# Optimization experiments

Hardware: AMD Instinct MI355X
Metric: run time of the kernel (lower is better)

## Reference

```python
import jax, jax.numpy as jnp
import numpy as np

N = 8192
E_DIM = 256
HID = 256
OUT = 128
N_PRED = 2_000_000


def setup_inputs() -> dict:
    key = jax.random.key(0)
    ks = jax.random.split(key, 6)
    node_indices = jnp.arange(N, dtype=jnp.int64) if jax.config.jax_enable_x64 else jnp.arange(N, dtype=jnp.int32)
    attn_matrix = jax.random.normal(ks[0], (N, N), dtype=jnp.float32)
    edge_label_index = jax.random.randint(ks[1], (2, N_PRED), 0, N)
    emb = jax.random.normal(ks[2], (N, E_DIM), dtype=jnp.float32) * 0.05
    W1 = jax.random.normal(ks[3], (E_DIM, HID), dtype=jnp.float32) * (1.0 / np.sqrt(E_DIM))
    b1 = jnp.zeros((HID,), dtype=jnp.float32)
    W2 = jax.random.normal(ks[4], (HID, OUT), dtype=jnp.float32) * (1.0 / np.sqrt(HID))
    b2 = jnp.zeros((OUT,), dtype=jnp.float32)
    return {"node_indices": node_indices, "attn_matrix": attn_matrix,
            "edge_label_index": edge_label_index, "emb": emb,
            "W1": W1, "b1": b1, "W2": W2, "b2": b2}


def reference(node_indices, attn_matrix, edge_label_index, emb, W1, b1, W2, b2):
    # dense_to_sparse of an (almost surely) all-nonzero dense matrix keeps all
    # N^2 edges (incl. diagonal), so no extra self-loops are added by gcn_norm.
    w = jax.nn.relu(attn_matrix)                       # edge weights after F.relu
    deg = w.sum(axis=0)                                # deg[j] = sum_i w[i,j] (scatter on col)
    dis = jnp.where(deg > 0, jax.lax.rsqrt(deg), 0.0)  # deg^{-1/2}, inf -> 0
    a_norm = dis[:, None] * w * dis[None, :]           # norm_ij = d_i^-1/2 w_ij d_j^-1/2

    x = emb[node_indices]                              # embedding lookup [N, E_DIM]
    # GCNConv: aggregate transformed features at target (col): out = A_norm^T @ (x W) + b
    h = jax.nn.relu(a_norm.T @ (x @ W1) + b1)          # [N, HID]
    z = a_norm.T @ (h @ W2) + b2                       # [N, OUT]

    # decode: dot product between endpoint embeddings
    scores = jnp.einsum('ed,ed->e', z[edge_label_index[0]], z[edge_label_index[1]])
    return scores
```

## Files before the change

kernel.cpp:

```cpp
#include <hip/hip_runtime.h>

typedef _Float16 half8  __attribute__((ext_vector_type(8)));
typedef _Float16 half4v __attribute__((ext_vector_type(4)));
typedef _Float16 half2v __attribute__((ext_vector_type(2)));
typedef float    floatx4 __attribute__((ext_vector_type(4)));
typedef float    f4v     __attribute__((ext_vector_type(4)));

#define NND 8192
#define PA  40
#define PT  128

__device__ __forceinline__ int swzk(int m, int k) { return k ^ (((m >> 3) & 3) << 3); }
__device__ __forceinline__ int swzT(int row, int chunk) { return chunk ^ ((row >> 2) & 15); }

#define GLOAD16(gp, lp) __builtin_amdgcn_global_load_lds(                        \
    (const __attribute__((address_space(1))) void*)(gp),                         \
    (__attribute__((address_space(3))) void*)(lp), 16, 0, 0)

#define VMCNT0() asm volatile("s_waitcnt vmcnt(0)" ::: "memory")

__device__ __forceinline__ float dis_of(float d) { return d > 0.f ? 1.f / sqrtf(d) : 0.f; }

__global__ __launch_bounds__(256) void k_degT(const float* __restrict__ A,
                                              _Float16* __restrict__ Wh,
                                              float* __restrict__ deg) {
    __shared__ _Float16 T[128 * PT];
    __shared__ float sdeg[8 * 128];
    int t  = threadIdx.x;
    int j0 = blockIdx.x * 128, i0 = blockIdx.y * 128;
    int c = t & 31;
    int g = t >> 5;

    f4v s = {0.f, 0.f, 0.f, 0.f};
    #pragma unroll
    for (int p = 0; p < 2; ++p) {
        int rb = 64 * p + 8 * g;
        f4v v[8];
        #pragma unroll
        for (int rr = 0; rr < 8; ++rr)
            v[rr] = *(const f4v*)(A + (size_t)(i0 + rb + rr) * NND + j0 + 4 * c);
        #pragma unroll
        for (int rr = 0; rr < 8; ++rr)
            #pragma unroll
            for (int u = 0; u < 4; ++u) v[rr][u] = fmaxf(v[rr][u], 0.f);
        #pragma unroll
        for (int u = 0; u < 4; ++u) {
            half8 hv;
            #pragma unroll
            for (int rr = 0; rr < 8; ++rr) { hv[rr] = (_Float16)v[rr][u]; s[u] += v[rr][u]; }
            int row = 4 * c + u;
            int chunk = 8 * p + g;
            *(half8*)(&T[row * PT + swzT(row, chunk) * 8]) = hv;
        }
    }
    *(f4v*)(&sdeg[g * 128 + 4 * c]) = s;
    __syncthreads();

    if (t < 128) {
        float d = 0.f;
        #pragma unroll
        for (int g2 = 0; g2 < 8; ++g2) d += sdeg[g2 * 128 + t];
        atomicAdd(&deg[j0 + t], d);
    }

    #pragma unroll
    for (int p = 0; p < 8; ++p) {
        int j  = 16 * p + (t >> 4);
        int mc = t & 15;
        half8 hv = *(const half8*)(&T[j * PT + swzT(j, mc) * 8]);
        *(half8*)(Wh + (size_t)(j0 + j) * NND + i0 + mc * 8) = hv;
    }
}

template <typename AT>
__global__ __launch_bounds__(256) void k_mm_small(
    const AT* __restrict__ Abase, const int* __restrict__ gather,
    const float* __restrict__ B, int NB,
    _Float16* __restrict__ outT, const float* __restrict__ deg, float out_scale) {

    __shared__ _Float16 As[128 * PA];
    __shared__ _Float16 Bs[64 * PA];

    int t  = threadIdx.x;
    int i0 = blockIdx.x * 128;
    int n0 = blockIdx.y * 64;

    int am = t & 127, akh = t >> 7;
    int row = i0 + am;
    if (gather) row = gather[row];
    const AT* arow = Abase + (size_t)row * 256;

    int tp = t & 15, kp = t >> 4;

    int lane = t & 63, w = t >> 6;
    int wm = w & 1, wn = w >> 1;
    int lm = lane & 15, q = lane >> 4;

    floatx4 acc[4][2];
    #pragma unroll
    for (int a = 0; a < 4; ++a)
        #pragma unroll
        for (int b = 0; b < 2; ++b) acc[a][b] = (floatx4){0.f, 0.f, 0.f, 0.f};

    for (int ks = 0; ks < 8; ++ks) {
        int c0 = ks * 32;

        half8 av[2];
        if constexpr (sizeof(AT) == 4) {
            #pragma unroll
            for (int cc = 0; cc < 2; ++cc) {
                f4v v0 = *(const f4v*)(arow + c0 + akh * 16 + cc * 8);
                f4v v1 = *(const f4v*)(arow + c0 + akh * 16 + cc * 8 + 4);
                half8 hv;
                #pragma unroll
                for (int e = 0; e < 4; ++e) {
                    hv[e]     = (_Float16)(16.f * v0[e]);
                    hv[4 + e] = (_Float16)(16.f * v1[e]);
                }
                av[cc] = hv;
            }
        } else {
            av[0] = *(const half8*)(arow + c0 + akh * 16);
            av[1] = *(const half8*)(arow + c0 + akh * 16 + 8);
        }

        const float* bp = B + (size_t)(c0 + 2 * kp) * NB + n0 + 4 * tp;
        f4v r0 = *(const f4v*)bp;
        f4v r1 = *(const f4v*)(bp + NB);

        __syncthreads();
        #pragma unroll
        for (int cc = 0; cc < 2; ++cc) {
            int k = akh * 16 + cc * 8;
            *(half8*)(&As[am * PA + swzk(am, k)]) = av[cc];
        }
        #pragma unroll
        for (int u = 0; u < 4; ++u) {
            int n = 4 * tp + u;
            half2v p = {(_Float16)r0[u], (_Float16)r1[u]};
            *(half2v*)(&Bs[n * PA + swzk(n, 2 * kp)]) = p;
        }
        __syncthreads();

        half8 af[4], bf[2];
        #pragma unroll
        for (int mt = 0; mt < 4; ++mt) {
            int m = wm * 64 + mt * 16 + lm;
            af[mt] = *(const half8*)(&As[m * PA + swzk(m, q * 8)]);
        }
        #pragma unroll
        for (int nt = 0; nt < 2; ++nt) {
            int n = wn * 32 + nt * 16 + lm;
            bf[nt] = *(const half8*)(&Bs[n * PA + swzk(n, q * 8)]);
        }
        #pragma unroll
        for (int mt = 0; mt < 4; ++mt)
            #pragma unroll
            for (int nt = 0; nt < 2; ++nt)
                acc[mt][nt] = __builtin_amdgcn_mfma_f32_16x16x32_f16(af[mt], bf[nt], acc[mt][nt], 0, 0, 0);
    }

    #pragma unroll
    for (int mt = 0; mt < 4; ++mt) {
        int ib = i0 + wm * 64 + mt * 16 + q * 4;
        float di[4];
        #pragma unroll
        for (int r = 0; r < 4; ++r) di[r] = dis_of(deg[ib + r]) * out_scale;
        #pragma unroll
        for (int nt = 0; nt < 2; ++nt) {
            int n = n0 + wn * 32 + nt * 16 + lm;
            #pragma unroll
            for (int r = 0; r < 4; ++r) {
                float v = acc[mt][nt][r] * di[r];
                outT[(size_t)n * NND + ib + r] = (_Float16)v;
            }
        }
    }
}

template <int BN, int ZSTEPS>
__global__ __launch_bounds__(256) void k_mm_big(
    const _Float16* __restrict__ Wh, const _Float16* __restrict__ Bt, float* __restrict__ Cp) {

    __shared__ __align__(16) _Float16 As[2 * 128 * 32];
    __shared__ __align__(16) _Float16 Bs[2 * 128 * 32];

    int t = threadIdx.x;
    int bx = blockIdx.x;
    bx = (bx & 7) * 8 + (bx >> 3);
    int j0 = bx * 128;
    int n0 = blockIdx.y * 128;
    size_t i_begin = (size_t)blockIdx.z * (ZSTEPS * 32);
    float* C = Cp + (size_t)blockIdx.z * (size_t)NND * BN;

    int lane = t & 63, w = t >> 6;
    int wm = w & 1, wn = w >> 1;
    int lm = lane & 15, q = lane >> 4;
    int qa = q ^ ((lm >> 1) & 3);

    int srow = lane >> 2;
    int scol = ((lane & 3) ^ ((lane >> 3) & 3)) * 8;
    const _Float16* aS0 = Wh + (size_t)(j0 + w * 16 + srow) * NND + i_begin + scol;
    const _Float16* aS1 = aS0 + (size_t)64 * NND;
    const _Float16* bS0 = Bt + (size_t)(n0 + w * 16 + srow) * NND + i_begin + scol;
    const _Float16* bS1 = bS0 + (size_t)64 * NND;

    char* aLb = (char*)As + w * 1024;
    char* bLb = (char*)Bs + w * 1024;

    floatx4 acc[4][4];
    #pragma unroll
    for (int a = 0; a < 4; ++a)
        #pragma unroll
        for (int b = 0; b < 4; ++b) acc[a][b] = (floatx4){0.f, 0.f, 0.f, 0.f};

    GLOAD16(aS0, aLb);
    GLOAD16(aS1, aLb + 4096);
    GLOAD16(bS0, bLb);
    GLOAD16(bS1, bLb + 4096);
    VMCNT0();
    __builtin_amdgcn_s_barrier();

    for (int ks = 0; ks < ZSTEPS; ++ks) {
        int cur = ks & 1;
        const _Float16* Ab = As + cur * 4096;
        const _Float16* Bb = Bs + cur * 4096;

        if (ks < ZSTEPS - 1) {
            int ko = (ks + 1) * 32;
            char* aL = aLb + (cur ^ 1) * 8192;
            char* bL = bLb + (cur ^ 1) * 8192;
            GLOAD16(aS0 + ko, aL);
            GLOAD16(aS1 + ko, aL + 4096);
            GLOAD16(bS0 + ko, bL);
            GLOAD16(bS1 + ko, bL + 4096);
        }

        half8 af[4], bf[4];
        #pragma unroll
        for (int mt = 0; mt < 4; ++mt) {
            int m = wm * 64 + mt * 16 + lm;
            af[mt] = *(const half8*)(&Ab[m * 32 + qa * 8]);
        }
        #pragma unroll
        for (int nt = 0; nt < 4; ++nt) {
            int n = wn * 64 + nt * 16 + lm;
            bf[nt] = *(const half8*)(&Bb[n * 32 + qa * 8]);
        }
        __builtin_amdgcn_s_setprio(1);
        #pragma unroll
        for (int mt = 0; mt < 4; ++mt)
            #pragma unroll
            for (int nt = 0; nt < 4; ++nt)
                acc[mt][nt] = __builtin_amdgcn_mfma_f32_16x16x32_f16(af[mt], bf[nt], acc[mt][nt], 0, 0, 0);
        __builtin_amdgcn_s_setprio(0);

        VMCNT0();
        __builtin_amdgcn_s_barrier();
    }

    #pragma unroll
    for (int mt = 0; mt < 4; ++mt) {
        int rb = j0 + wm * 64 + mt * 16 + q * 4;
        #pragma unroll
        for (int nt = 0; nt < 4; ++nt) {
            int col = n0 + wn * 64 + nt * 16 + lm;
            #pragma unroll
            for (int r = 0; r < 4; ++r)
                C[(size_t)(rb + r) * BN + col] = acc[mt][nt][r];
        }
    }
}

template <int NSH, bool RELU, int NZ>
__global__ __launch_bounds__(256) void k_finalize(const float* __restrict__ Cp, const float* __restrict__ deg,
                                                  const float* __restrict__ bias, _Float16* __restrict__ out) {
    int idx4 = (blockIdx.x * 256 + threadIdx.x) * 4;
    f4v v = {0.f, 0.f, 0.f, 0.f};
    #pragma unroll
    for (int z = 0; z < NZ; ++z) {
        f4v p = *(const f4v*)(Cp + (size_t)z * (NND << NSH) + idx4);
        #pragma unroll
        for (int r = 0; r < 4; ++r) v[r] += p[r];
    }
    int j  = idx4 >> NSH;
    int n0 = idx4 & ((1 << NSH) - 1);
    float dj = dis_of(deg[j]) * (1.f / 1024.f);
    f4v b4 = *(const f4v*)(bias + n0);
    half4v o;
    #pragma unroll
    for (int r = 0; r < 4; ++r) {
        float x = v[r] * dj + b4[r];
        if (RELU) x = fmaxf(x, 0.f);
        o[r] = (_Float16)(x * 64.f);
    }
    *(half4v*)(out + idx4) = o;
}

__global__ __launch_bounds__(256) void k_edges(const _Float16* __restrict__ zh, const int* __restrict__ ei,
                                               float* __restrict__ out, int npred) {
    int g0 = ((blockIdx.x * 256 + threadIdx.x) >> 4) * 4;
    int l = threadIdx.x & 15;
    #pragma unroll
    for (int e = 0; e < 4; ++e) {
        int g = g0 + e;
        if (g >= npred) return;
        int a = ei[g], b = ei[npred + g];
        half8 za = *(const half8*)(zh + (size_t)a * 128 + l * 8);
        half8 zb = *(const half8*)(zh + (size_t)b * 128 + l * 8);
        float s = 0.f;
        #pragma unroll
        for (int u = 0; u < 4; ++u) {
            half2v a2 = {za[2 * u], za[2 * u + 1]};
            half2v b2 = {zb[2 * u], zb[2 * u + 1]};
            s = __builtin_amdgcn_fdot2(a2, b2, s, false);
        }
        s += __shfl_xor(s, 1);
        s += __shfl_xor(s, 2);
        s += __shfl_xor(s, 4);
        s += __shfl_xor(s, 8);
        if (l == 0) out[g] = s * (1.f / 4096.f);
    }
}

extern "C" void kernel_launch(void* const* d_in, const int* in_sizes, int n_in,
                              void* d_out, int out_size, void* d_ws, size_t ws_size,
                              hipStream_t stream) {
    const int*   nodes = (const int*)d_in[0];
    const float* attn  = (const float*)d_in[1];
    const int*   eidx  = (const int*)d_in[2];
    const float* emb   = (const float*)d_in[3];
    const float* W1    = (const float*)d_in[4];
    const float* b1    = (const float*)d_in[5];
    const float* W2    = (const float*)d_in[6];
    const float* b2    = (const float*)d_in[7];
    float* out = (float*)d_out;
    int npred = in_sizes[2] / 2;

    char* ws = (char*)d_ws;
    float*    deg = (float*)(ws);
    _Float16* Wh  = (_Float16*)(ws + 0x10000);
    float*    C1p = (float*)(ws + 0x8010000);
    float*    C2p = (float*)(ws + 0xC010000);
    _Float16* M1p = (_Float16*)(ws + 0xE010000);
    _Float16* h   = (_Float16*)(ws + 0xE410000);
    _Float16* M2p = (_Float16*)(ws + 0xE810000);
    _Float16* zh  = (_Float16*)(ws + 0xEA10000);

    hipMemsetAsync(deg, 0, 8192 * sizeof(float), stream);

    k_degT<<<dim3(64, 64), 256, 0, stream>>>(attn, Wh, deg);

    k_mm_small<float><<<dim3(64, 4), 256, 0, stream>>>(emb, nodes, W1, 256, M1p, deg, 64.f);
    k_mm_big<256, 64><<<dim3(64, 2, 4), 256, 0, stream>>>(Wh, M1p, C1p);
    k_finalize<8, true, 4><<<2048, 256, 0, stream>>>(C1p, deg, b1, h);
    k_mm_small<_Float16><<<dim3(64, 2), 256, 0, stream>>>(h, nullptr, W2, 128, M2p, deg, 16.f);
    k_mm_big<128, 32><<<dim3(64, 1, 8), 256, 0, stream>>>(Wh, M2p, C2p);
    k_finalize<7, false, 8><<<1024, 256, 0, stream>>>(C2p, deg, b2, zh);

    k_edges<<<(npred + 63) / 64, 256, 0, stream>>>(zh, eidx, out, npred);
}
```

Baseline: 607.5 us.

## Widen first GEMM N-tile to full width, add nontemporal hints, batch edge gathers

The first big GEMM now covers the full 256-wide output in one block (NT=8) instead of two y-blocks, so the fp16 adjacency matrix is streamed once rather than twice. To keep the GPU filled it uses 8 K-splits instead of 4, and the finalize kernel is adjusted to match. Partial-sum stores and loads, plus edge index and output traffic, are marked nontemporal. The edge decoder issues all index and embedding gathers before computing, to increase memory-level parallelism. In exchange, this raises register pressure (128 accumulator registers per thread) and doubles the partial-sum buffer traffic for the first layer.

```diff
diff --git a/kernel.cpp b/kernel.cpp
--- a/kernel.cpp
+++ b/kernel.cpp
@@ -178,18 +178,20 @@
     }
 }
 
-template <int BN, int ZSTEPS>
-__global__ __launch_bounds__(256) void k_mm_big(
+template <int BN, int NT, int ZSTEPS>
+__global__ __launch_bounds__(256, 2) void k_mm_big(
     const _Float16* __restrict__ Wh, const _Float16* __restrict__ Bt, float* __restrict__ Cp) {
 
+    constexpr int BISS = BN / 64;
+    constexpr int ABYT = 128 * 32 * 2;
+    constexpr int BBYT = BN * 32 * 2;
     __shared__ __align__(16) _Float16 As[2 * 128 * 32];
-    __shared__ __align__(16) _Float16 Bs[2 * 128 * 32];
+    __shared__ __align__(16) _Float16 Bs[2 * BN * 32];
 
     int t = threadIdx.x;
     int bx = blockIdx.x;
     bx = (bx & 7) * 8 + (bx >> 3);
     int j0 = bx * 128;
-    int n0 = blockIdx.y * 128;
     size_t i_begin = (size_t)blockIdx.z * (ZSTEPS * 32);
     float* C = Cp + (size_t)blockIdx.z * (size_t)NND * BN;
 
@@ -200,58 +202,56 @@
 
     int srow = lane >> 2;
     int scol = ((lane & 3) ^ ((lane >> 3) & 3)) * 8;
-    const _Float16* aS0 = Wh + (size_t)(j0 + w * 16 + srow) * NND + i_begin + scol;
-    const _Float16* aS1 = aS0 + (size_t)64 * NND;
-    const _Float16* bS0 = Bt + (size_t)(n0 + w * 16 + srow) * NND + i_begin + scol;
-    const _Float16* bS1 = bS0 + (size_t)64 * NND;
+    const _Float16* aS = Wh + (size_t)(j0 + w * 16 + srow) * NND + i_begin + scol;
+    const _Float16* bS = Bt + (size_t)(w * 16 + srow) * NND + i_begin + scol;
 
     char* aLb = (char*)As + w * 1024;
     char* bLb = (char*)Bs + w * 1024;
 
-    floatx4 acc[4][4];
+    floatx4 acc[4][NT];
     #pragma unroll
     for (int a = 0; a < 4; ++a)
         #pragma unroll
-        for (int b = 0; b < 4; ++b) acc[a][b] = (floatx4){0.f, 0.f, 0.f, 0.f};
-
-    GLOAD16(aS0, aLb);
-    GLOAD16(aS1, aLb + 4096);
-    GLOAD16(bS0, bLb);
-    GLOAD16(bS1, bLb + 4096);
+        for (int b = 0; b < NT; ++b) acc[a][b] = (floatx4){0.f, 0.f, 0.f, 0.f};
+
+    #pragma unroll
+    for (int s = 0; s < 2; ++s)    GLOAD16(aS + (size_t)(64 * s) * NND, aLb + s * 4096);
+    #pragma unroll
+    for (int s = 0; s < BISS; ++s) GLOAD16(bS + (size_t)(64 * s) * NND, bLb + s * 4096);
     VMCNT0();
     __builtin_amdgcn_s_barrier();
 
     for (int ks = 0; ks < ZSTEPS; ++ks) {
         int cur = ks & 1;
-        const _Float16* Ab = As + cur * 4096;
-        const _Float16* Bb = Bs + cur * 4096;
+        const _Float16* Ab = As + cur * (128 * 32);
+        const _Float16* Bb = Bs + cur * (BN * 32);
 
         if (ks < ZSTEPS - 1) {
             int ko = (ks + 1) * 32;
-            char* aL = aLb + (cur ^ 1) * 8192;
-            char* bL = bLb + (cur ^ 1) * 8192;
-            GLOAD16(aS0 + ko, aL);
-            GLOAD16(aS1 + ko, aL + 4096);
-            GLOAD16(bS0 + ko, bL);
-            GLOAD16(bS1 + ko, bL + 4096);
-        }
-
-        half8 af[4], bf[4];
+            char* aL = aLb + (cur ^ 1) * ABYT;
+            char* bL = bLb + (cur ^ 1) * BBYT;
+            #pragma unroll
+            for (int s = 0; s < 2; ++s)    GLOAD16(aS + (size_t)(64 * s) * NND + ko, aL + s * 4096);
+            #pragma unroll
+            for (int s = 0; s < BISS; ++s) GLOAD16(bS + (size_t)(64 * s) * NND + ko, bL + s * 4096);
+        }
+
+        half8 af[4], bf[NT];
         #pragma unroll
         for (int mt = 0; mt < 4; ++mt) {
             int m = wm * 64 + mt * 16 + lm;
             af[mt] = *(const half8*)(&Ab[m * 32 + qa * 8]);
         }
         #pragma unroll
-        for (int nt = 0; nt < 4; ++nt) {
-            int n = wn * 64 + nt * 16 + lm;
+        for (int nt = 0; nt < NT; ++nt) {
+            int n = wn * (NT * 16) + nt * 16 + lm;
             bf[nt] = *(const half8*)(&Bb[n * 32 + qa * 8]);
         }
         __builtin_amdgcn_s_setprio(1);
         #pragma unroll
         for (int mt = 0; mt < 4; ++mt)
             #pragma unroll
-            for (int nt = 0; nt < 4; ++nt)
+            for (int nt = 0; nt < NT; ++nt)
                 acc[mt][nt] = __builtin_amdgcn_mfma_f32_16x16x32_f16(af[mt], bf[nt], acc[mt][nt], 0, 0, 0);
         __builtin_amdgcn_s_setprio(0);
 
@@ -263,11 +263,11 @@
     for (int mt = 0; mt < 4; ++mt) {
         int rb = j0 + wm * 64 + mt * 16 + q * 4;
         #pragma unroll
-        for (int nt = 0; nt < 4; ++nt) {
-            int col = n0 + wn * 64 + nt * 16 + lm;
+        for (int nt = 0; nt < NT; ++nt) {
+            int col = wn * (NT * 16) + nt * 16 + lm;
             #pragma unroll
             for (int r = 0; r < 4; ++r)
-                C[(size_t)(rb + r) * BN + col] = acc[mt][nt][r];
+                __builtin_nontemporal_store(acc[mt][nt][r], &C[(size_t)(rb + r) * BN + col]);
         }
     }
 }
@@ -279,7 +279,7 @@
     f4v v = {0.f, 0.f, 0.f, 0.f};
     #pragma unroll
     for (int z = 0; z < NZ; ++z) {
-        f4v p = *(const f4v*)(Cp + (size_t)z * (NND << NSH) + idx4);
+        f4v p = __builtin_nontemporal_load((const f4v*)(Cp + (size_t)z * (NND << NSH) + idx4));
         #pragma unroll
         for (int r = 0; r < 4; ++r) v[r] += p[r];
     }
@@ -301,25 +301,33 @@
                                                float* __restrict__ out, int npred) {
     int g0 = ((blockIdx.x * 256 + threadIdx.x) >> 4) * 4;
     int l = threadIdx.x & 15;
+    if (g0 >= npred) return;
+    int a[4], b[4];
     #pragma unroll
     for (int e = 0; e < 4; ++e) {
-        int g = g0 + e;
-        if (g >= npred) return;
-        int a = ei[g], b = ei[npred + g];
-        half8 za = *(const half8*)(zh + (size_t)a * 128 + l * 8);
-        half8 zb = *(const half8*)(zh + (size_t)b * 128 + l * 8);
+        a[e] = __builtin_nontemporal_load(ei + g0 + e);
+        b[e] = __builtin_nontemporal_load(ei + npred + g0 + e);
+    }
+    half8 za[4], zb[4];
+    #pragma unroll
+    for (int e = 0; e < 4; ++e) {
+        za[e] = *(const half8*)(zh + (size_t)a[e] * 128 + l * 8);
+        zb[e] = *(const half8*)(zh + (size_t)b[e] * 128 + l * 8);
+    }
+    #pragma unroll
+    for (int e = 0; e < 4; ++e) {
         float s = 0.f;
         #pragma unroll
         for (int u = 0; u < 4; ++u) {
-            half2v a2 = {za[2 * u], za[2 * u + 1]};
-            half2v b2 = {zb[2 * u], zb[2 * u + 1]};
+            half2v a2 = {za[e][2 * u], za[e][2 * u + 1]};
+            half2v b2 = {zb[e][2 * u], zb[e][2 * u + 1]};
             s = __builtin_amdgcn_fdot2(a2, b2, s, false);
         }
         s += __shfl_xor(s, 1);
         s += __shfl_xor(s, 2);
         s += __shfl_xor(s, 4);
         s += __shfl_xor(s, 8);
-        if (l == 0) out[g] = s * (1.f / 4096.f);
+        if (l == 0) __builtin_nontemporal_store(s * (1.f / 4096.f), out + g0 + e);
     }
 }
 
@@ -352,10 +360,10 @@
     k_degT<<<dim3(64, 64), 256, 0, stream>>>(attn, Wh, deg);
 
     k_mm_small<float><<<dim3(64, 4), 256, 0, stream>>>(emb, nodes, W1, 256, M1p, deg, 64.f);
-    k_mm_big<256, 64><<<dim3(64, 2, 4), 256, 0, stream>>>(Wh, M1p, C1p);
-    k_finalize<8, true, 4><<<2048, 256, 0, stream>>>(C1p, deg, b1, h);
+    k_mm_big<256, 8, 32><<<dim3(64, 1, 8), 256, 0, stream>>>(Wh, M1p, C1p);
+    k_finalize<8, true, 8><<<2048, 256, 0, stream>>>(C1p, deg, b1, h);
     k_mm_small<_Float16><<<dim3(64, 2), 256, 0, stream>>>(h, nullptr, W2, 128, M2p, deg, 16.f);
-    k_mm_big<128, 32><<<dim3(64, 1, 8), 256, 0, stream>>>(Wh, M2p, C2p);
+    k_mm_big<128, 4, 32><<<dim3(64, 1, 8), 256, 0, stream>>>(Wh, M2p, C2p);
     k_finalize<7, false, 8><<<1024, 256, 0, stream>>>(C2p, deg, b2, zh);
 
     k_edges<<<(npred + 63) / 64, 256, 0, stream>>>(zh, eidx, out, npred);
```

Result: faster. 588.2 us (-3.2%).
